# Optimization experiments

Hardware: AMD Instinct MI355X
Metric: run time of the kernel (lower is better)

Reference implementation:

```python
import jax, jax.numpy as jnp
import numpy as np

N_NODES = 50000
N_EDGES = 800000
D_MODEL = 128
N_HEADS = 8
D_HEAD = D_MODEL // N_HEADS


def _layernorm(x, g, b, eps=1e-5):
    mu = jnp.mean(x, axis=-1, keepdims=True)
    var = jnp.mean(jnp.square(x - mu), axis=-1, keepdims=True)
    return (x - mu) * jax.lax.rsqrt(var + eps) * g + b


def setup_inputs() -> dict:
    key = jax.random.key(0)
    ks = jax.random.split(key, 8)
    x = jax.random.normal(ks[0], (N_NODES, D_MODEL), dtype=jnp.float32)
    edge_attr = jax.random.normal(ks[1], (N_EDGES, N_HEADS, D_HEAD), dtype=jnp.float32)
    s = 1.0 / np.sqrt(D_MODEL)
    qkv_w = jax.random.normal(ks[2], (D_MODEL, 3 * D_MODEL), dtype=jnp.float32) * s
    qkv_b = jax.random.normal(ks[3], (3 * D_MODEL,), dtype=jnp.float32) * 0.01
    out_w = jax.random.normal(ks[4], (D_MODEL, D_MODEL), dtype=jnp.float32) * s
    out_b = jax.random.normal(ks[5], (D_MODEL,), dtype=jnp.float32) * 0.01
    ln_g = jnp.ones((D_MODEL,), dtype=jnp.float32)
    ln_b = jnp.zeros((D_MODEL,), dtype=jnp.float32)
    edge_index = jax.random.randint(ks[6], (2, N_EDGES), 0, N_NODES, dtype=jnp.int64)
    return {"x": x, "edge_attr": edge_attr, "qkv_w": qkv_w, "qkv_b": qkv_b,
            "out_w": out_w, "out_b": out_b, "ln_g": ln_g, "ln_b": ln_b,
            "edge_index": edge_index}


def reference(x, edge_attr, qkv_w, qkv_b, out_w, out_b, ln_g, ln_b, edge_index):
    N, C = x.shape
    h = _layernorm(x, ln_g, ln_b)  # pre-norm
    qkv = (h @ qkv_w + qkv_b).reshape(N, 3, N_HEADS, D_HEAD)
    q, k, v = qkv[:, 0], qkv[:, 1], qkv[:, 2]  # each [N, H, D]
    src, dst = edge_index[0], edge_index[1]    # PyG: j = source, i = target
    # edge-wise attention logits [E, H]
    scores = jnp.sum(q[dst] * (k[src] + edge_attr), axis=-1) * (D_HEAD ** -0.5)
    # segment softmax over target index
    m = jax.ops.segment_max(scores, dst, num_segments=N)          # [N, H]
    m = jnp.where(jnp.isfinite(m), m, 0.0)
    e = jnp.exp(scores - m[dst])                                   # [E, H]
    s = jax.ops.segment_sum(e, dst, num_segments=N)                # [N, H]
    attn = e / jnp.maximum(s[dst], 1e-16)                          # [E, H]
    msg = v[src] * attn[:, :, None]                                # [E, H, D]
    agg = jax.ops.segment_sum(msg, dst, num_segments=N)            # [N, H, D]
    out = agg.reshape(N, C) @ out_w + out_b
    return x + out
```

## Files before the change

kernel.cpp:

```cpp
#include <hip/hip_runtime.h>

#define NN 50000
#define NE 800000

__global__ __launch_bounds__(256) void ln_kernel(
    const float* __restrict__ x, const float* __restrict__ g,
    const float* __restrict__ b, float* __restrict__ h, int n) {
  int wid  = (blockIdx.x * blockDim.x + threadIdx.x) >> 6;
  int lane = threadIdx.x & 63;
  if (wid >= n) return;
  const float2 v = *(const float2*)(x + (size_t)wid * 128 + lane * 2);
  float sum = v.x + v.y;
  float sq  = v.x * v.x + v.y * v.y;
#pragma unroll
  for (int off = 32; off > 0; off >>= 1) {
    sum += __shfl_down(sum, off);
    sq  += __shfl_down(sq, off);
  }
  sum = __shfl(sum, 0);
  sq  = __shfl(sq, 0);
  float mu  = sum * (1.f / 128.f);
  float var = sq * (1.f / 128.f) - mu * mu;
  float inv = rsqrtf(var + 1e-5f);
  float2 gg = *(const float2*)(g + lane * 2);
  float2 bb = *(const float2*)(b + lane * 2);
  float2 o;
  o.x = (v.x - mu) * inv * gg.x + bb.x;
  o.y = (v.y - mu) * inv * gg.y + bb.y;
  *(float2*)(h + (size_t)wid * 128 + lane * 2) = o;
}

__global__ __launch_bounds__(256) void gemm128(
    const float* __restrict__ A, const float* __restrict__ W,
    const float* __restrict__ bias, const float* __restrict__ resid,
    float* __restrict__ Out, int M, int Nw) {
  __shared__ float As[128][65];
  __shared__ float Bs[64][64];

  int tid = threadIdx.x;
  int ty  = tid >> 4;
  int tx  = tid & 15;
  int m0  = blockIdx.x * 128;
  int n0  = blockIdx.y * 64;

  float acc[8][4] = {};

  for (int kb = 0; kb < 128; kb += 64) {
#pragma unroll
    for (int i = 0; i < 8; ++i) {
      int c = tid + i * 256;
      int row = c >> 4, kv = c & 15;
      float4 av = make_float4(0.f, 0.f, 0.f, 0.f);
      if (m0 + row < M)
        av = *(const float4*)(A + (size_t)(m0 + row) * 128 + kb + kv * 4);
      As[row][kv * 4 + 0] = av.x;
      As[row][kv * 4 + 1] = av.y;
      As[row][kv * 4 + 2] = av.z;
      As[row][kv * 4 + 3] = av.w;
    }
#pragma unroll
    for (int i = 0; i < 4; ++i) {
      int c = tid + i * 256;
      int kr = c >> 4, nv = c & 15;
      float4 bv = *(const float4*)(W + (size_t)(kb + kr) * Nw + n0 + nv * 4);
      *(float4*)&Bs[kr][nv * 4] = bv;
    }
    __syncthreads();
#pragma unroll
    for (int k = 0; k < 64; ++k) {
      float4 bv = *(float4*)&Bs[k][tx * 4];
#pragma unroll
      for (int j = 0; j < 8; ++j) {
        float a = As[ty * 8 + j][k];
        acc[j][0] += a * bv.x;
        acc[j][1] += a * bv.y;
        acc[j][2] += a * bv.z;
        acc[j][3] += a * bv.w;
      }
    }
    __syncthreads();
  }

  float4 bb = *(const float4*)(bias + n0 + tx * 4);
#pragma unroll
  for (int j = 0; j < 8; ++j) {
    int row = m0 + ty * 8 + j;
    if (row < M) {
      float4 o;
      o.x = acc[j][0] + bb.x;
      o.y = acc[j][1] + bb.y;
      o.z = acc[j][2] + bb.z;
      o.w = acc[j][3] + bb.w;
      if (resid) {
        float4 r = *(const float4*)(resid + (size_t)row * Nw + n0 + tx * 4);
        o.x += r.x; o.y += r.y; o.z += r.z; o.w += r.w;
      }
      *(float4*)(Out + (size_t)row * Nw + n0 + tx * 4) = o;
    }
  }
}

__global__ __launch_bounds__(256) void count_kernel(
    const int* __restrict__ ei, int* __restrict__ cnt, int E) {
  int e = blockIdx.x * blockDim.x + threadIdx.x;
  if (e >= E) return;
  atomicAdd(&cnt[ei[E + e]], 1);
}

__global__ __launch_bounds__(1024) void scan_kernel(
    const int* __restrict__ cnt, int* __restrict__ row_start, int n) {
  __shared__ int sums[1024];
  int tid = threadIdx.x;
  const int CH = (n + 1023) / 1024;
  int begin = tid * CH;
  int end   = min(begin + CH, n);
  int s = 0;
  for (int i = begin; i < end; ++i) s += cnt[i];
  sums[tid] = s;
  __syncthreads();
  for (int off = 1; off < 1024; off <<= 1) {
    int t = (tid >= off) ? sums[tid - off] : 0;
    __syncthreads();
    if (tid >= off) sums[tid] += t;
    __syncthreads();
  }
  int run = sums[tid] - s;
  for (int i = begin; i < end; ++i) {
    row_start[i] = run;
    run += cnt[i];
  }
  if (tid == 1023) row_start[n] = run;
}

__global__ __launch_bounds__(256) void scatter_kernel(
    const int* __restrict__ ei, int* __restrict__ cursor,
    int* __restrict__ perm, int E) {
  int e = blockIdx.x * blockDim.x + threadIdx.x;
  if (e >= E) return;
  int pos = atomicAdd(&cursor[ei[E + e]], 1);
  perm[pos] = e;
}

__global__ __launch_bounds__(256) void fused_attn(
    const float* __restrict__ qkv, const float* __restrict__ edge_attr,
    const int* __restrict__ ei, const int* __restrict__ row_start,
    const int* __restrict__ perm, float* __restrict__ agg, int N, int E) {
  int node = (blockIdx.x * blockDim.x + threadIdx.x) >> 6;
  if (node >= N) return;
  int lane = threadIdx.x & 63;
  int hg   = lane >> 3;
  int sub  = lane & 7;
  int ch   = hg * 16 + sub * 2;

  float2 q2 = *(const float2*)(qkv + (size_t)node * 384 + ch);

  float m = -INFINITY, l = 0.f;
  float2 acc = make_float2(0.f, 0.f);

  int beg  = row_start[node];
  int stop = row_start[node + 1];
  for (int i = beg; i < stop; ++i) {
    int e   = perm[i];
    int src = ei[e];
    float2 kv = *(const float2*)(qkv + (size_t)src * 384 + 128 + ch);
    float2 ea = *(const float2*)(edge_attr + (size_t)e * 128 + ch);
    float p = q2.x * (kv.x + ea.x) + q2.y * (kv.y + ea.y);
    p += __shfl_xor(p, 1);
    p += __shfl_xor(p, 2);
    p += __shfl_xor(p, 4);
    float s  = p * 0.25f;
    float mn = fmaxf(m, s);
    float scale = __expf(m - mn);
    float pe    = __expf(s - mn);
    l = l * scale + pe;
    float2 vv = *(const float2*)(qkv + (size_t)src * 384 + 256 + ch);
    acc.x = acc.x * scale + pe * vv.x;
    acc.y = acc.y * scale + pe * vv.y;
    m = mn;
  }
  float inv = 1.f / fmaxf(l, 1e-16f);
  float2 o = make_float2(acc.x * inv, acc.y * inv);
  *(float2*)(agg + (size_t)node * 128 + ch) = o;
}

extern "C" void kernel_launch(void* const* d_in, const int* in_sizes, int n_in,
                              void* d_out, int out_size, void* d_ws,
                              size_t ws_size, hipStream_t stream) {
  const float* x         = (const float*)d_in[0];
  const float* edge_attr = (const float*)d_in[1];
  const float* qkv_w     = (const float*)d_in[2];
  const float* qkv_b     = (const float*)d_in[3];
  const float* out_w     = (const float*)d_in[4];
  const float* out_b     = (const float*)d_in[5];
  const float* ln_g      = (const float*)d_in[6];
  const float* ln_b      = (const float*)d_in[7];
  const int*   ei        = (const int*)d_in[8];
  float* out = (float*)d_out;

  const int N = NN, E = NE;
  float* h         = (float*)d_ws;
  float* qkv       = h + (size_t)N * 128;
  int*   cnt       = (int*)(qkv + (size_t)N * 384);
  int*   row_start = cnt + N;
  int*   cursor    = row_start + N + 1;
  int*   perm      = cursor + N;
  float* agg       = h;

  hipMemsetAsync(cnt, 0, (size_t)N * 4, stream);
  count_kernel<<<(E + 255) / 256, 256, 0, stream>>>(ei, cnt, E);
  scan_kernel<<<1, 1024, 0, stream>>>(cnt, row_start, N);
  hipMemcpyAsync(cursor, row_start, (size_t)N * 4, hipMemcpyDeviceToDevice,
                 stream);
  scatter_kernel<<<(E + 255) / 256, 256, 0, stream>>>(ei, cursor, perm, E);

  ln_kernel<<<(N * 64 + 255) / 256, 256, 0, stream>>>(x, ln_g, ln_b, h, N);

  dim3 g1((N + 127) / 128, 384 / 64);
  gemm128<<<g1, 256, 0, stream>>>(h, qkv_w, qkv_b, nullptr, qkv, N, 384);

  fused_attn<<<(N * 64 + 255) / 256, 256, 0, stream>>>(
      qkv, edge_attr, ei, row_start, perm, agg, N, E);

  dim3 g2((N + 127) / 128, 128 / 64);
  gemm128<<<g2, 256, 0, stream>>>(agg, out_w, out_b, x, out, N, 128);
}
```

Baseline: 979.9 us.

## Rewrite GEMMs as row-per-thread with broadcast weights; unroll attention edge loop by two

Replaces the shared-memory tiled GEMM with a kernel where each thread owns one output row and 64 accumulators. It streams A from global memory and reads weights through wave-uniform broadcast loads, with no LDS and no barriers. The fused attention loop now processes two edges per iteration, issuing both gathers up front to raise memory-level parallelism. The risk is that per-thread A loads are uncoalesced and the 64-element accumulator raises register pressure.

```diff
diff --git a/kernel.cpp b/kernel.cpp
--- a/kernel.cpp
+++ b/kernel.cpp
@@ -30,72 +30,61 @@
   *(float2*)(h + (size_t)wid * 128 + lane * 2) = o;
 }
 
-__global__ __launch_bounds__(256) void gemm128(
+__global__ __launch_bounds__(256) void gemm_rw(
     const float* __restrict__ A, const float* __restrict__ W,
     const float* __restrict__ bias, const float* __restrict__ resid,
     float* __restrict__ Out, int M, int Nw) {
-  __shared__ float As[128][65];
-  __shared__ float Bs[64][64];
-
-  int tid = threadIdx.x;
-  int ty  = tid >> 4;
-  int tx  = tid & 15;
-  int m0  = blockIdx.x * 128;
-  int n0  = blockIdx.y * 64;
-
-  float acc[8][4] = {};
-
-  for (int kb = 0; kb < 128; kb += 64) {
-#pragma unroll
-    for (int i = 0; i < 8; ++i) {
-      int c = tid + i * 256;
-      int row = c >> 4, kv = c & 15;
-      float4 av = make_float4(0.f, 0.f, 0.f, 0.f);
-      if (m0 + row < M)
-        av = *(const float4*)(A + (size_t)(m0 + row) * 128 + kb + kv * 4);
-      As[row][kv * 4 + 0] = av.x;
-      As[row][kv * 4 + 1] = av.y;
-      As[row][kv * 4 + 2] = av.z;
-      As[row][kv * 4 + 3] = av.w;
-    }
-#pragma unroll
-    for (int i = 0; i < 4; ++i) {
-      int c = tid + i * 256;
-      int kr = c >> 4, nv = c & 15;
-      float4 bv = *(const float4*)(W + (size_t)(kb + kr) * Nw + n0 + nv * 4);
-      *(float4*)&Bs[kr][nv * 4] = bv;
-    }
-    __syncthreads();
-#pragma unroll
-    for (int k = 0; k < 64; ++k) {
-      float4 bv = *(float4*)&Bs[k][tx * 4];
-#pragma unroll
-      for (int j = 0; j < 8; ++j) {
-        float a = As[ty * 8 + j][k];
-        acc[j][0] += a * bv.x;
-        acc[j][1] += a * bv.y;
-        acc[j][2] += a * bv.z;
-        acc[j][3] += a * bv.w;
+  int row  = blockIdx.x * 256 + threadIdx.x;
+  int n0   = blockIdx.y * 64;
+  bool live = row < M;
+  const float* Ar = A + (size_t)(live ? row : 0) * 128;
+
+  float acc[64];
+#pragma unroll
+  for (int j = 0; j < 64; ++j) acc[j] = 0.f;
+
+  for (int k = 0; k < 128; k += 4) {
+    float4 a4 = *(const float4*)(Ar + k);
+#pragma unroll
+    for (int t = 0; t < 4; ++t) {
+      float ak = (t == 0) ? a4.x : (t == 1) ? a4.y : (t == 2) ? a4.z : a4.w;
+      const float* wr = W + (size_t)(k + t) * Nw + n0;
+#pragma unroll
+      for (int j = 0; j < 16; ++j) {
+        float4 w = *(const float4*)(wr + 4 * j);
+        acc[4 * j + 0] += ak * w.x;
+        acc[4 * j + 1] += ak * w.y;
+        acc[4 * j + 2] += ak * w.z;
+        acc[4 * j + 3] += ak * w.w;
       }
     }
-    __syncthreads();
-  }
-
-  float4 bb = *(const float4*)(bias + n0 + tx * 4);
-#pragma unroll
-  for (int j = 0; j < 8; ++j) {
-    int row = m0 + ty * 8 + j;
-    if (row < M) {
-      float4 o;
-      o.x = acc[j][0] + bb.x;
-      o.y = acc[j][1] + bb.y;
-      o.z = acc[j][2] + bb.z;
-      o.w = acc[j][3] + bb.w;
-      if (resid) {
-        float4 r = *(const float4*)(resid + (size_t)row * Nw + n0 + tx * 4);
-        o.x += r.x; o.y += r.y; o.z += r.z; o.w += r.w;
-      }
-      *(float4*)(Out + (size_t)row * Nw + n0 + tx * 4) = o;
+  }
+
+  if (!live) return;
+  float* o = Out + (size_t)row * Nw + n0;
+  if (resid) {
+    const float* r = resid + (size_t)row * Nw + n0;
+#pragma unroll
+    for (int j = 0; j < 16; ++j) {
+      float4 bb = *(const float4*)(bias + n0 + 4 * j);
+      float4 rv = *(const float4*)(r + 4 * j);
+      float4 ov;
+      ov.x = acc[4 * j + 0] + bb.x + rv.x;
+      ov.y = acc[4 * j + 1] + bb.y + rv.y;
+      ov.z = acc[4 * j + 2] + bb.z + rv.z;
+      ov.w = acc[4 * j + 3] + bb.w + rv.w;
+      *(float4*)(o + 4 * j) = ov;
+    }
+  } else {
+#pragma unroll
+    for (int j = 0; j < 16; ++j) {
+      float4 bb = *(const float4*)(bias + n0 + 4 * j);
+      float4 ov;
+      ov.x = acc[4 * j + 0] + bb.x;
+      ov.y = acc[4 * j + 1] + bb.y;
+      ov.z = acc[4 * j + 2] + bb.z;
+      ov.w = acc[4 * j + 3] + bb.w;
+      *(float4*)(o + 4 * j) = ov;
     }
   }
 }
@@ -148,9 +137,7 @@
   int node = (blockIdx.x * blockDim.x + threadIdx.x) >> 6;
   if (node >= N) return;
   int lane = threadIdx.x & 63;
-  int hg   = lane >> 3;
-  int sub  = lane & 7;
-  int ch   = hg * 16 + sub * 2;
+  int ch   = lane * 2;
 
   float2 q2 = *(const float2*)(qkv + (size_t)node * 384 + ch);
 
@@ -159,7 +146,36 @@
 
   int beg  = row_start[node];
   int stop = row_start[node + 1];
-  for (int i = beg; i < stop; ++i) {
+  int i = beg;
+  for (; i + 2 <= stop; i += 2) {
+    int e0 = perm[i], e1 = perm[i + 1];
+    int s0 = ei[e0], s1 = ei[e1];
+    float2 k0 = *(const float2*)(qkv + (size_t)s0 * 384 + 128 + ch);
+    float2 k1 = *(const float2*)(qkv + (size_t)s1 * 384 + 128 + ch);
+    float2 a0 = *(const float2*)(edge_attr + (size_t)e0 * 128 + ch);
+    float2 a1 = *(const float2*)(edge_attr + (size_t)e1 * 128 + ch);
+    float2 v0 = *(const float2*)(qkv + (size_t)s0 * 384 + 256 + ch);
+    float2 v1 = *(const float2*)(qkv + (size_t)s1 * 384 + 256 + ch);
+    float p0 = q2.x * (k0.x + a0.x) + q2.y * (k0.y + a0.y);
+    float p1 = q2.x * (k1.x + a1.x) + q2.y * (k1.y + a1.y);
+    p0 += __shfl_xor(p0, 1);
+    p1 += __shfl_xor(p1, 1);
+    p0 += __shfl_xor(p0, 2);
+    p1 += __shfl_xor(p1, 2);
+    p0 += __shfl_xor(p0, 4);
+    p1 += __shfl_xor(p1, 4);
+    float sc0 = p0 * 0.25f;
+    float sc1 = p1 * 0.25f;
+    float mn = fmaxf(fmaxf(m, sc0), sc1);
+    float scale = __expf(m - mn);
+    float pe0   = __expf(sc0 - mn);
+    float pe1   = __expf(sc1 - mn);
+    l = l * scale + pe0 + pe1;
+    acc.x = acc.x * scale + pe0 * v0.x + pe1 * v1.x;
+    acc.y = acc.y * scale + pe0 * v0.y + pe1 * v1.y;
+    m = mn;
+  }
+  if (i < stop) {
     int e   = perm[i];
     int src = ei[e];
     float2 kv = *(const float2*)(qkv + (size_t)src * 384 + 128 + ch);
@@ -215,12 +231,12 @@
 
   ln_kernel<<<(N * 64 + 255) / 256, 256, 0, stream>>>(x, ln_g, ln_b, h, N);
 
-  dim3 g1((N + 127) / 128, 384 / 64);
-  gemm128<<<g1, 256, 0, stream>>>(h, qkv_w, qkv_b, nullptr, qkv, N, 384);
+  dim3 g1((N + 255) / 256, 384 / 64);
+  gemm_rw<<<g1, 256, 0, stream>>>(h, qkv_w, qkv_b, nullptr, qkv, N, 384);
 
   fused_attn<<<(N * 64 + 255) / 256, 256, 0, stream>>>(
       qkv, edge_attr, ei, row_start, perm, agg, N, E);
 
-  dim3 g2((N + 127) / 128, 128 / 64);
-  gemm128<<<g2, 256, 0, stream>>>(agg, out_w, out_b, x, out, N, 128);
-}
+  dim3 g2((N + 255) / 256, 128 / 64);
+  gemm_rw<<<g2, 256, 0, stream>>>(agg, out_w, out_b, x, out, N, 128);
+}
```

New measurement: 956.9 us. 2.3% less time.
